# Kernel tuning notes

Measured on AMD Instinct MI355X. Metric: run time of the kernel, lower is better.

Reference implementation:

```python
import jax, jax.numpy as jnp
import numpy as np

EPS = 1e-5  # config.layer_norm_epsilon


def setup_inputs() -> dict:
    key = jax.random.key(0)
    ks = jax.random.split(key, 7)
    B, S, D, K = 16, 2048, 768, 64
    return {
        "x": jax.random.normal(ks[0], (B, S, D), dtype=jnp.float32),
        "W_up": jax.random.normal(ks[1], (D, K), dtype=jnp.float32) * 0.02,
        "b_up": jax.random.normal(ks[2], (D,), dtype=jnp.float32) * 0.02,
        "W_down": jax.random.normal(ks[3], (K, D), dtype=jnp.float32) * 0.02,
        "b_down": jax.random.normal(ks[4], (K,), dtype=jnp.float32) * 0.02,
        "W_ln": 1.0 + 0.02 * jax.random.normal(ks[5], (D,), dtype=jnp.float32),
        "b_ln": 0.02 * jax.random.normal(ks[6], (D,), dtype=jnp.float32),
    }


def reference(x, W_up, b_up, W_down, b_down, W_ln, b_ln):
    # F.layer_norm with normalized_shape = x.size()[1:] -> normalize jointly
    # over (S, D) per batch element; W_ln/b_ln (shape [D]) broadcast to (S, D).
    mu = jnp.mean(x, axis=(1, 2), keepdims=True)            # [B,1,1]
    var = jnp.mean(jnp.square(x - mu), axis=(1, 2), keepdims=True)
    xn = (x - mu) * jax.lax.rsqrt(var + EPS) * W_ln + b_ln  # [B,S,D]
    # down-proj (no bias) -> ReLU -> up-proj (no bias) -> residual add
    h = jax.nn.relu(jnp.einsum('bsd,kd->bsk', xn, W_down))  # [B,S,K]
    return x + jnp.einsum('bsk,dk->bsd', h, W_up)           # [B,S,D]
```

## Files before the change

### kernel.cpp

```cpp
#include <hip/hip_runtime.h>

#define EPS   1e-5f
#define NB    16
#define NS    2048
#define ND    768
#define NK    64
#define NPB   (NS * ND)

typedef __attribute__((ext_vector_type(8))) short short8;
typedef __attribute__((ext_vector_type(4))) float f32x4;

static __device__ __forceinline__ short f2bf(float f) {
    unsigned u = __builtin_bit_cast(unsigned, f);
    u += 0x7fffu + ((u >> 16) & 1u);
    return (short)(u >> 16);
}

__global__ __launch_bounds__(256) void prep_reduce(
    const float* __restrict__ x, const float* __restrict__ W_up,
    const float* __restrict__ W_down, const float* __restrict__ W_ln,
    const float* __restrict__ b_ln, float2* __restrict__ stats_p,
    float* __restrict__ c1, float* __restrict__ c2,
    short* __restrict__ wdp, short* __restrict__ wub)
{
    __shared__ float red[8];
    const int bid = blockIdx.x, tid = threadIdx.x;
    const int wid = tid >> 6, lane = tid & 63;

    if (bid < 1024) {
        const int b = bid >> 6;
        const int chunk = bid & 63;
        const f32x4* xv = (const f32x4*)(x + (size_t)b * NPB + (size_t)chunk * (NPB / 64));
        float s = 0.f, ss = 0.f;
        #pragma unroll 8
        for (int i = tid; i < NPB / 64 / 4; i += 256) {
            f32x4 v = xv[i];
            s  += v[0] + v[1] + v[2] + v[3];
            ss += v[0]*v[0] + v[1]*v[1] + v[2]*v[2] + v[3]*v[3];
        }
        #pragma unroll
        for (int off = 32; off > 0; off >>= 1) {
            s  += __shfl_down(s, off, 64);
            ss += __shfl_down(ss, off, 64);
        }
        if (lane == 0) stats_p[bid * 4 + wid] = make_float2(s, ss);
    } else if (bid < 1088) {
        const int k = bid - 1024;
        float pc1 = 0.f, pc2 = 0.f;
        #pragma unroll
        for (int d = tid; d < ND; d += 256) {
            float wl = W_ln[d], wd = W_down[k * ND + d], bl = b_ln[d];
            wdp[k * ND + d] = f2bf(wl * wd);
            pc1 += wl * wd;
            pc2 += bl * wd;
        }
        #pragma unroll
        for (int off = 32; off > 0; off >>= 1) {
            pc1 += __shfl_down(pc1, off, 64);
            pc2 += __shfl_down(pc2, off, 64);
        }
        if (lane == 0) { red[wid] = pc1; red[4 + wid] = pc2; }
        __syncthreads();
        if (tid == 0) c1[k] = red[0] + red[1] + red[2] + red[3];
        if (tid == 1) c2[k] = red[4] + red[5] + red[6] + red[7];
    } else {
        const int i = (bid - 1088) * 256 + tid;
        wub[i] = f2bf(W_up[i]);
    }
}

__global__ __launch_bounds__(256) void fused_main(
    const float* __restrict__ x, const short* __restrict__ wdp,
    const short* __restrict__ wub, const float* __restrict__ c1,
    const float* __restrict__ c2, const float2* __restrict__ stats_p,
    float* __restrict__ out)
{
    __shared__ __align__(16) char  wbuf[49152];
    __shared__ __align__(16) short h_lds[4][1024];
    __shared__ __align__(16) float stg[4][1088];

    const int tid  = threadIdx.x;
    const int wid  = tid >> 6;
    const int lane = tid & 63;
    const int r    = lane & 15;
    const int g    = lane >> 4;
    const int sw   = (r & 7) << 4;
    const int row0 = blockIdx.x * 64 + wid * 16;
    const int b    = blockIdx.x >> 5;

    float s = 0.f, ss = 0.f;
    #pragma unroll
    for (int i = 0; i < 4; ++i) {
        float2 sp = stats_p[b * 256 + i * 64 + lane];
        s += sp.x; ss += sp.y;
    }
    #pragma unroll
    for (int off = 32; off > 0; off >>= 1) {
        s  += __shfl_xor(s, off, 64);
        ss += __shfl_xor(ss, off, 64);
    }
    const float invN = 1.f / (float)NPB;
    const float mu  = s * invN;
    const float var = ss * invN - mu * mu;
    const float rs  = rsqrtf(var + EPS);

    auto stage_wdp = [&](int c, int p) {
        char* dst = wbuf + p * 24576;
        #pragma unroll
        for (int i = 0; i < 6; ++i) {
            int idx = i * 256 + tid;
            int row = idx / 24, u = idx % 24;
            short8 v = *(const short8*)(wdp + row * ND + c * 192 + u * 8);
            *(short8*)(dst + row * 384 + ((u * 16) ^ ((row & 7) << 4))) = v;
        }
    };
    auto stage_wub = [&](int w, int p) {
        char* dst = wbuf + p * 16384;
        #pragma unroll
        for (int i = 0; i < 4; ++i) {
            int idx = i * 256 + tid;
            int row = idx >> 3, u = idx & 7;
            short8 v = *(const short8*)(wub + (w * 128 + row) * 64 + u * 8);
            *(short8*)(dst + row * 128 + ((u * 16) ^ ((row & 7) << 4))) = v;
        }
    };

    f32x4 acc[4] = {};
    auto compute_g1 = [&](int p, int c) {
        const char* B = wbuf + p * 24576;
        const float* xa = x + (size_t)(row0 + r) * ND + c * 192 + g * 8;
        #pragma unroll
        for (int kk = 0; kk < 6; ++kk) {
            f32x4 a0 = *(const f32x4*)(xa + kk * 32);
            f32x4 a1 = *(const f32x4*)(xa + kk * 32 + 4);
            short8 af;
            af[0] = f2bf(a0[0]); af[1] = f2bf(a0[1]); af[2] = f2bf(a0[2]); af[3] = f2bf(a0[3]);
            af[4] = f2bf(a1[0]); af[5] = f2bf(a1[1]); af[6] = f2bf(a1[2]); af[7] = f2bf(a1[3]);
            #pragma unroll
            for (int cf = 0; cf < 4; ++cf) {
                short8 bf = *(const short8*)(B + (cf * 16 + r) * 384
                                               + ((kk * 64 + g * 16) ^ sw));
                acc[cf] = __builtin_amdgcn_mfma_f32_16x16x32_bf16(af, bf, acc[cf], 0, 0, 0);
            }
        }
    };

    stage_wdp(0, 0);                  __syncthreads();
    stage_wdp(1, 1); compute_g1(0, 0); __syncthreads();
    stage_wdp(2, 0); compute_g1(1, 1); __syncthreads();
    stage_wdp(3, 1); compute_g1(0, 2); __syncthreads();
    stage_wub(0, 0); compute_g1(1, 3); __syncthreads();

    #pragma unroll
    for (int cf = 0; cf < 4; ++cf) {
        const int col = cf * 16 + r;
        const float kb = c2[col] - rs * mu * c1[col];
        #pragma unroll
        for (int reg = 0; reg < 4; ++reg) {
            float z = fmaf(rs, acc[cf][reg], kb);
            const int hrow = g * 4 + reg;
            *(short*)((char*)h_lds[wid] + hrow * 128
                      + ((col * 2) ^ ((hrow & 7) << 4))) = f2bf(fmaxf(z, 0.f));
        }
    }

    const char* H = (const char*)h_lds[wid] + r * 128;
    short8 a2_0 = *(const short8*)(H + ((g * 16) ^ sw));
    short8 a2_1 = *(const short8*)(H + ((64 + g * 16) ^ sw));

    const float* xr   = x   + (size_t)row0 * ND;
    float*       outr = out + (size_t)row0 * ND;
    const int erow = lane >> 4;
    const int ecol = (lane & 15) * 4;
    float* S = stg[wid];

    for (int w = 0; w < 6; ++w) {
        if (w < 5) stage_wub(w + 1, (w + 1) & 1);
        const char* W = wbuf + (w & 1) * 16384;
        #pragma unroll
        for (int dq = 0; dq < 2; ++dq) {
            const int dcg = w * 2 + dq;
            f32x4 acc2[4] = {};
            #pragma unroll
            for (int cf = 0; cf < 4; ++cf) {
                const int dl = dq * 64 + cf * 16 + r;
                short8 b0 = *(const short8*)(W + dl * 128 + ((g * 16) ^ sw));
                short8 b1 = *(const short8*)(W + dl * 128 + ((64 + g * 16) ^ sw));
                acc2[cf] = __builtin_amdgcn_mfma_f32_16x16x32_bf16(a2_0, b0, acc2[cf], 0, 0, 0);
                acc2[cf] = __builtin_amdgcn_mfma_f32_16x16x32_bf16(a2_1, b1, acc2[cf], 0, 0, 0);
            }
            #pragma unroll
            for (int cf = 0; cf < 4; ++cf)
                #pragma unroll
                for (int reg = 0; reg < 4; ++reg)
                    S[(g * 4 + reg) * 68 + cf * 16 + r] = acc2[cf][reg];
            #pragma unroll
            for (int j = 0; j < 4; ++j) {
                const int row = j * 4 + erow;
                f32x4 v  = *(const f32x4*)(S + row * 68 + ecol);
                const int col = dcg * 64 + ecol;
                f32x4 xv = *(const f32x4*)(xr + (size_t)row * ND + col);
                v[0] += xv[0]; v[1] += xv[1]; v[2] += xv[2]; v[3] += xv[3];
                __builtin_nontemporal_store(v[0], &outr[(size_t)row * ND + col]);
                __builtin_nontemporal_store(v[1], &outr[(size_t)row * ND + col + 1]);
                __builtin_nontemporal_store(v[2], &outr[(size_t)row * ND + col + 2]);
                __builtin_nontemporal_store(v[3], &outr[(size_t)row * ND + col + 3]);
            }
        }
        __syncthreads();
    }
}

extern "C" void kernel_launch(void* const* d_in, const int* in_sizes, int n_in,
                              void* d_out, int out_size, void* d_ws, size_t ws_size,
                              hipStream_t stream)
{
    const float* x      = (const float*)d_in[0];
    const float* W_up   = (const float*)d_in[1];
    const float* W_down = (const float*)d_in[3];
    const float* W_ln   = (const float*)d_in[5];
    const float* b_ln   = (const float*)d_in[6];
    float* out = (float*)d_out;

    char* ws = (char*)d_ws;
    float2* stats_p = (float2*)ws;
    float*  c1      = (float*)(ws + 32768);
    float*  c2      = (float*)(ws + 33024);
    short*  wdp     = (short*)(ws + 33280);
    short*  wub     = (short*)(ws + 131584);

    prep_reduce<<<1280, 256, 0, stream>>>(x, W_up, W_down, W_ln, b_ln,
                                          stats_p, c1, c2, wdp, wub);
    fused_main<<<512, 256, 0, stream>>>(x, wdp, wub, c1, c2, stats_p, out);
}
```

Before: 65.64 us.

## Stage x tiles through LDS as bf16 and vectorize output stores

The first GEMM now stages each 192-column chunk of x into LDS as bf16 with coalesced row loads. Previously each lane read strided fragments straight from global memory. The W_down chunks are loaded into a single buffer with a sync per chunk, which drops the previous double-buffered overlap of staging and compute. All LDS buffers are merged into one aliased 73KB array, and the four scalar nontemporal stores become one vector store. The larger LDS footprint and the serialized staging may cut occupancy and lose the compute/load overlap.

```diff
diff --git a/kernel.cpp b/kernel.cpp
--- a/kernel.cpp
+++ b/kernel.cpp
@@ -75,9 +75,7 @@
     const float* __restrict__ c2, const float2* __restrict__ stats_p,
     float* __restrict__ out)
 {
-    __shared__ __align__(16) char  wbuf[49152];
-    __shared__ __align__(16) short h_lds[4][1024];
-    __shared__ __align__(16) float stg[4][1088];
+    __shared__ __align__(16) char lds[74752];
 
     const int tid  = threadIdx.x;
     const int wid  = tid >> 6;
@@ -85,7 +83,7 @@
     const int r    = lane & 15;
     const int g    = lane >> 4;
     const int sw   = (r & 7) << 4;
-    const int row0 = blockIdx.x * 64 + wid * 16;
+    const int row0 = blockIdx.x * 64;
     const int b    = blockIdx.x >> 5;
 
     float s = 0.f, ss = 0.f;
@@ -104,8 +102,8 @@
     const float var = ss * invN - mu * mu;
     const float rs  = rsqrtf(var + EPS);
 
-    auto stage_wdp = [&](int c, int p) {
-        char* dst = wbuf + p * 24576;
+    auto stage_wdp = [&](int c) {
+        char* dst = lds;
         #pragma unroll
         for (int i = 0; i < 6; ++i) {
             int idx = i * 256 + tid;
@@ -114,8 +112,23 @@
             *(short8*)(dst + row * 384 + ((u * 16) ^ ((row & 7) << 4))) = v;
         }
     };
+    auto stage_x = [&](int c) {
+        char* dst = lds + 24576;
+        #pragma unroll
+        for (int i = 0; i < 6; ++i) {
+            int idx = i * 256 + tid;
+            int row = idx / 24, u = idx % 24;
+            const float* src = x + (size_t)(row0 + row) * ND + c * 192 + u * 8;
+            f32x4 a0 = *(const f32x4*)(src);
+            f32x4 a1 = *(const f32x4*)(src + 4);
+            short8 h8;
+            h8[0]=f2bf(a0[0]); h8[1]=f2bf(a0[1]); h8[2]=f2bf(a0[2]); h8[3]=f2bf(a0[3]);
+            h8[4]=f2bf(a1[0]); h8[5]=f2bf(a1[1]); h8[6]=f2bf(a1[2]); h8[7]=f2bf(a1[3]);
+            *(short8*)(dst + row * 384 + ((u * 16) ^ ((row & 7) << 4))) = h8;
+        }
+    };
     auto stage_wub = [&](int w, int p) {
-        char* dst = wbuf + p * 16384;
+        char* dst = lds + p * 16384;
         #pragma unroll
         for (int i = 0; i < 4; ++i) {
             int idx = i * 256 + tid;
@@ -126,31 +139,30 @@
     };
 
     f32x4 acc[4] = {};
-    auto compute_g1 = [&](int p, int c) {
-        const char* B = wbuf + p * 24576;
-        const float* xa = x + (size_t)(row0 + r) * ND + c * 192 + g * 8;
-        #pragma unroll
-        for (int kk = 0; kk < 6; ++kk) {
-            f32x4 a0 = *(const f32x4*)(xa + kk * 32);
-            f32x4 a1 = *(const f32x4*)(xa + kk * 32 + 4);
-            short8 af;
-            af[0] = f2bf(a0[0]); af[1] = f2bf(a0[1]); af[2] = f2bf(a0[2]); af[3] = f2bf(a0[3]);
-            af[4] = f2bf(a1[0]); af[5] = f2bf(a1[1]); af[6] = f2bf(a1[2]); af[7] = f2bf(a1[3]);
-            #pragma unroll
-            for (int cf = 0; cf < 4; ++cf) {
-                short8 bf = *(const short8*)(B + (cf * 16 + r) * 384
-                                               + ((kk * 64 + g * 16) ^ sw));
-                acc[cf] = __builtin_amdgcn_mfma_f32_16x16x32_bf16(af, bf, acc[cf], 0, 0, 0);
+    for (int c = 0; c < 4; ++c) {
+        stage_wdp(c);
+        stage_x(c);
+        __syncthreads();
+        {
+            const char* B = lds;
+            const char* X = lds + 24576;
+            const int arow = wid * 16 + r;
+            #pragma unroll
+            for (int kk = 0; kk < 6; ++kk) {
+                short8 af = *(const short8*)(X + arow * 384 + ((kk * 64 + g * 16) ^ sw));
+                #pragma unroll
+                for (int cf = 0; cf < 4; ++cf) {
+                    short8 bf = *(const short8*)(B + (cf * 16 + r) * 384
+                                                   + ((kk * 64 + g * 16) ^ sw));
+                    acc[cf] = __builtin_amdgcn_mfma_f32_16x16x32_bf16(af, bf, acc[cf], 0, 0, 0);
+                }
             }
         }
-    };
-
-    stage_wdp(0, 0);                  __syncthreads();
-    stage_wdp(1, 1); compute_g1(0, 0); __syncthreads();
-    stage_wdp(2, 0); compute_g1(1, 1); __syncthreads();
-    stage_wdp(3, 1); compute_g1(0, 2); __syncthreads();
-    stage_wub(0, 0); compute_g1(1, 3); __syncthreads();
-
+        __syncthreads();
+    }
+
+    stage_wub(0, 0);
+    char* H = lds + 66560 + wid * 2048;
     #pragma unroll
     for (int cf = 0; cf < 4; ++cf) {
         const int col = cf * 16 + r;
@@ -159,24 +171,23 @@
         for (int reg = 0; reg < 4; ++reg) {
             float z = fmaf(rs, acc[cf][reg], kb);
             const int hrow = g * 4 + reg;
-            *(short*)((char*)h_lds[wid] + hrow * 128
-                      + ((col * 2) ^ ((hrow & 7) << 4))) = f2bf(fmaxf(z, 0.f));
-        }
-    }
-
-    const char* H = (const char*)h_lds[wid] + r * 128;
-    short8 a2_0 = *(const short8*)(H + ((g * 16) ^ sw));
-    short8 a2_1 = *(const short8*)(H + ((64 + g * 16) ^ sw));
-
-    const float* xr   = x   + (size_t)row0 * ND;
-    float*       outr = out + (size_t)row0 * ND;
+            *(short*)(H + hrow * 128 + ((col * 2) ^ ((hrow & 7) << 4))) = f2bf(fmaxf(z, 0.f));
+        }
+    }
+    __syncthreads();
+
+    short8 a2_0 = *(const short8*)(H + r * 128 + ((g * 16) ^ sw));
+    short8 a2_1 = *(const short8*)(H + r * 128 + ((64 + g * 16) ^ sw));
+
+    const float* xr   = x   + (size_t)(row0 + wid * 16) * ND;
+    float*       outr = out + (size_t)(row0 + wid * 16) * ND;
     const int erow = lane >> 4;
     const int ecol = (lane & 15) * 4;
-    float* S = stg[wid];
+    float* S = (float*)(lds + 49152) + wid * 1088;
 
     for (int w = 0; w < 6; ++w) {
         if (w < 5) stage_wub(w + 1, (w + 1) & 1);
-        const char* W = wbuf + (w & 1) * 16384;
+        const char* W = lds + (w & 1) * 16384;
         #pragma unroll
         for (int dq = 0; dq < 2; ++dq) {
             const int dcg = w * 2 + dq;
@@ -201,10 +212,7 @@
                 const int col = dcg * 64 + ecol;
                 f32x4 xv = *(const f32x4*)(xr + (size_t)row * ND + col);
                 v[0] += xv[0]; v[1] += xv[1]; v[2] += xv[2]; v[3] += xv[3];
-                __builtin_nontemporal_store(v[0], &outr[(size_t)row * ND + col]);
-                __builtin_nontemporal_store(v[1], &outr[(size_t)row * ND + col + 1]);
-                __builtin_nontemporal_store(v[2], &outr[(size_t)row * ND + col + 2]);
-                __builtin_nontemporal_store(v[3], &outr[(size_t)row * ND + col + 3]);
+                __builtin_nontemporal_store(v, (f32x4*)(outr + (size_t)row * ND + col));
             }
         }
         __syncthreads();
```

Result: no change. 66.22 us (+0.9%).

## Split weight staging into register prefetch and deferred LDS write with lgkm-only barriers

Applied to the files above, without the earlier changes.

Weight tile staging is split into a global-to-register load issued before compute and an LDS write issued after compute, so global load latency overlaps the MFMA work. __syncthreads is replaced by a barrier that waits only on LDS counters, so outstanding global stores and loads are not drained at each barrier. The residual output store is also turned into a single vectorized nontemporal store. The cost is higher register pressure from holding prefetched tiles across compute, which could lower occupancy.

```diff
diff --git a/kernel.cpp b/kernel.cpp
--- a/kernel.cpp
+++ b/kernel.cpp
@@ -9,6 +9,12 @@
 
 typedef __attribute__((ext_vector_type(8))) short short8;
 typedef __attribute__((ext_vector_type(4))) float f32x4;
+
+#define LGKM_BAR() do {                                      \
+    asm volatile("s_waitcnt lgkmcnt(0)" ::: "memory");       \
+    __builtin_amdgcn_sched_barrier(0);                       \
+    __builtin_amdgcn_s_barrier();                            \
+} while (0)
 
 static __device__ __forceinline__ short f2bf(float f) {
     unsigned u = __builtin_bit_cast(unsigned, f);
@@ -104,24 +110,38 @@
     const float var = ss * invN - mu * mu;
     const float rs  = rsqrtf(var + EPS);
 
-    auto stage_wdp = [&](int c, int p) {
+    auto wdp_load = [&](int c, short8* v) {
+        #pragma unroll
+        for (int i = 0; i < 6; ++i) {
+            int idx = i * 256 + tid;
+            int row = idx / 24, u = idx % 24;
+            v[i] = *(const short8*)(wdp + row * ND + c * 192 + u * 8);
+        }
+    };
+    auto wdp_write = [&](int p, const short8* v) {
         char* dst = wbuf + p * 24576;
         #pragma unroll
         for (int i = 0; i < 6; ++i) {
             int idx = i * 256 + tid;
             int row = idx / 24, u = idx % 24;
-            short8 v = *(const short8*)(wdp + row * ND + c * 192 + u * 8);
-            *(short8*)(dst + row * 384 + ((u * 16) ^ ((row & 7) << 4))) = v;
-        }
-    };
-    auto stage_wub = [&](int w, int p) {
+            *(short8*)(dst + row * 384 + ((u * 16) ^ ((row & 7) << 4))) = v[i];
+        }
+    };
+    auto wub_load = [&](int w, short8* v) {
+        #pragma unroll
+        for (int i = 0; i < 4; ++i) {
+            int idx = i * 256 + tid;
+            int row = idx >> 3, u = idx & 7;
+            v[i] = *(const short8*)(wub + (w * 128 + row) * 64 + u * 8);
+        }
+    };
+    auto wub_write = [&](int p, const short8* v) {
         char* dst = wbuf + p * 16384;
         #pragma unroll
         for (int i = 0; i < 4; ++i) {
             int idx = i * 256 + tid;
             int row = idx >> 3, u = idx & 7;
-            short8 v = *(const short8*)(wub + (w * 128 + row) * 64 + u * 8);
-            *(short8*)(dst + row * 128 + ((u * 16) ^ ((row & 7) << 4))) = v;
+            *(short8*)(dst + row * 128 + ((u * 16) ^ ((row & 7) << 4))) = v[i];
         }
     };
 
@@ -145,11 +165,31 @@
         }
     };
 
-    stage_wdp(0, 0);                  __syncthreads();
-    stage_wdp(1, 1); compute_g1(0, 0); __syncthreads();
-    stage_wdp(2, 0); compute_g1(1, 1); __syncthreads();
-    stage_wdp(3, 1); compute_g1(0, 2); __syncthreads();
-    stage_wub(0, 0); compute_g1(1, 3); __syncthreads();
+    {
+        short8 v[6];
+        wdp_load(0, v); wdp_write(0, v);
+    }
+    LGKM_BAR();
+    {
+        short8 v[6];
+        wdp_load(1, v); compute_g1(0, 0); wdp_write(1, v);
+    }
+    LGKM_BAR();
+    {
+        short8 v[6];
+        wdp_load(2, v); compute_g1(1, 1); wdp_write(0, v);
+    }
+    LGKM_BAR();
+    {
+        short8 v[6];
+        wdp_load(3, v); compute_g1(0, 2); wdp_write(1, v);
+    }
+    LGKM_BAR();
+    {
+        short8 u[4];
+        wub_load(0, u); compute_g1(1, 3); wub_write(0, u);
+    }
+    LGKM_BAR();
 
     #pragma unroll
     for (int cf = 0; cf < 4; ++cf) {
@@ -175,7 +215,8 @@
     float* S = stg[wid];
 
     for (int w = 0; w < 6; ++w) {
-        if (w < 5) stage_wub(w + 1, (w + 1) & 1);
+        short8 u[4];
+        if (w < 5) wub_load(w + 1, u);
         const char* W = wbuf + (w & 1) * 16384;
         #pragma unroll
         for (int dq = 0; dq < 2; ++dq) {
@@ -201,13 +242,11 @@
                 const int col = dcg * 64 + ecol;
                 f32x4 xv = *(const f32x4*)(xr + (size_t)row * ND + col);
                 v[0] += xv[0]; v[1] += xv[1]; v[2] += xv[2]; v[3] += xv[3];
-                __builtin_nontemporal_store(v[0], &outr[(size_t)row * ND + col]);
-                __builtin_nontemporal_store(v[1], &outr[(size_t)row * ND + col + 1]);
-                __builtin_nontemporal_store(v[2], &outr[(size_t)row * ND + col + 2]);
-                __builtin_nontemporal_store(v[3], &outr[(size_t)row * ND + col + 3]);
+                __builtin_nontemporal_store(v, (f32x4*)(outr + (size_t)row * ND + col));
             }
         }
-        __syncthreads();
+        if (w < 5) wub_write((w + 1) & 1, u);
+        LGKM_BAR();
     }
 }
 
```

Measured after the change: 66.83 us. No clear change (+1.8%).
